# Performance work log

Measured on AMD Instinct MI355X. Metric: run time of the kernel, lower is better.

Reference implementation:

```python
import jax, jax.numpy as jnp
import numpy as np
from jax import lax

DN = ('NCHW', 'OIHW', 'NCHW')


def _conv(x, w, groups, pad):
    return lax.conv_general_dilated(x, w, (1, 1), ((pad, pad), (pad, pad)),
                                    dimension_numbers=DN, feature_group_count=groups)


def setup_inputs() -> dict:
    key = jax.random.key(0)
    k0, k1, k2, k3, k4 = jax.random.split(key, 5)
    B, C, H, W, O = 8, 192, 56, 56, 384
    x = jax.random.normal(k0, (B, C, H, W), jnp.float32)
    # torch init: normal(0, sqrt(2/n)), n = kh*kw*out_ch
    og_dw = jax.random.normal(k1, (C, 1, 3, 3), jnp.float32) * np.sqrt(2.0 / (9 * C))
    og_pw = jax.random.normal(k2, (18, C, 1, 1), jnp.float32) * np.sqrt(2.0 / 18)
    dcn_w = jax.random.normal(k3, (C, 1, 3, 3), jnp.float32) * np.sqrt(2.0 / (9 * C))
    pw_w = jax.random.normal(k4, (O, C, 1, 1), jnp.float32) * np.sqrt(2.0 / O)
    return {'x': x, 'og_dw': og_dw, 'og_pw': og_pw, 'dcn_w': dcn_w, 'pw_w': pw_w}


def _deform_sample(x, dy, dx):
    # x: [B,C,H,W]; dy,dx: [B,9,H,W] learned offsets. Returns [B,C,9,H,W]
    B, C, H, W = x.shape
    ky = (jnp.repeat(jnp.arange(3), 3) - 1).astype(x.dtype)   # tap row offsets
    kx = (jnp.tile(jnp.arange(3), 3) - 1).astype(x.dtype)     # tap col offsets
    gh = jnp.arange(H, dtype=x.dtype)[:, None]
    gw = jnp.arange(W, dtype=x.dtype)[None, :]
    ys = gh[None, None] + ky[None, :, None, None] + dy        # [B,9,H,W]
    xs = gw[None, None] + kx[None, :, None, None] + dx
    y0 = jnp.floor(ys)
    x0 = jnp.floor(xs)
    ty = ys - y0
    tx = xs - x0
    y0i = y0.astype(jnp.int32)
    x0i = x0.astype(jnp.int32)
    xf = x.reshape(B, C, H * W)
    gather = jax.vmap(lambda xb, ib: xb[:, ib])  # ([C,HW],[9,H,W]) -> [C,9,H,W]
    val = jnp.zeros((B, C, 9, H, W), x.dtype)
    corners = [(y0i, x0i, (1 - ty) * (1 - tx)),
               (y0i, x0i + 1, (1 - ty) * tx),
               (y0i + 1, x0i, ty * (1 - tx)),
               (y0i + 1, x0i + 1, ty * tx)]
    for yi, xi, wgt in corners:
        valid = ((yi >= 0) & (yi < H) & (xi >= 0) & (xi < W)).astype(x.dtype)
        idx = jnp.clip(yi, 0, H - 1) * W + jnp.clip(xi, 0, W - 1)  # [B,9,H,W]
        v = gather(xf, idx)                                        # [B,C,9,H,W]
        val = val + v * (wgt * valid)[:, None]
    return val


def reference(x, og_dw, og_pw, dcn_w, pw_w):
    B, C, H, W = x.shape
    O = pw_w.shape[0]
    # offset generator: depthwise 3x3 then 1x1 -> 18 channels, clamped
    off = _conv(_conv(x, og_dw, C, 1), og_pw, 1, 0)
    off = jnp.clip(off, -1.0, 1.0)
    off = off.reshape(B, 9, 2, H, W)
    dy, dx = off[:, :, 0], off[:, :, 1]
    # depthwise deformable conv 3x3
    val = _deform_sample(x, dy, dx)                       # [B,C,9,H,W]
    y = jnp.einsum('bckhw,ck->bchw', val, dcn_w.reshape(C, 9))
    # pointwise conv + Hardswish
    y = jnp.einsum('bchw,oc->bohw', y, pw_w.reshape(O, C))
    return y * jnp.clip(y + 3.0, 0.0, 6.0) / 6.0
```

## Files before the change

### kernel.cpp

```cpp
#include <hip/hip_runtime.h>

#define TPB 256
constexpr int B_ = 8, C_ = 192, H_ = 56, W_ = 56, O_ = 384;
constexpr int HW_ = H_ * W_;
constexpr int NOFF = 18;
constexpr int NPIX = B_ * HW_;
constexpr int K2 = 9 * C_;

typedef __attribute__((ext_vector_type(8))) short short8v;
typedef __attribute__((ext_vector_type(4))) float f32x4;

__device__ inline unsigned short f2bf(float f) {
  unsigned u = __builtin_bit_cast(unsigned, f);
  unsigned r = (u + 0x7fffu + ((u >> 16) & 1u)) >> 16;
  return (unsigned short)r;
}
__device__ inline float bflo(unsigned u) {
  return __builtin_bit_cast(float, u << 16);
}
__device__ inline float bfhi(unsigned u) {
  return __builtin_bit_cast(float, u & 0xffff0000u);
}

__global__ __launch_bounds__(TPB) void k_prep(const float* __restrict__ og_dw,
                                              const float* __restrict__ og_pw,
                                              const float* __restrict__ pw,
                                              unsigned short* __restrict__ wtb,
                                              unsigned short* __restrict__ w2b) {
  int i = blockIdx.x * TPB + threadIdx.x;
  if (i < O_ * C_) wtb[i] = f2bf(pw[i]);
  int j = i - O_ * C_;
  if (j >= 0 && j < 32 * K2) {
    int o = j / K2, k = j - o * K2;
    int tap = k / C_, c = k - tap * C_;
    float v = 0.f;
    if (o < NOFF) v = og_pw[o * C_ + c] * og_dw[c * 9 + tap];
    w2b[j] = f2bf(v);
  }
}

__global__ __launch_bounds__(TPB) void k_xt(const float* __restrict__ x,
                                            unsigned short* __restrict__ xt) {
  __shared__ unsigned short tile[64 * 198];
  int tid = threadIdx.x;
  int P0 = blockIdx.x * 64;
  int b = blockIdx.y;
#pragma unroll
  for (int i = 0; i < 48; ++i) {
    int idx = i * TPB + tid;
    int px = idx & 63;
    int c = idx >> 6;
    float v = x[((size_t)(b * C_ + c)) * HW_ + P0 + px];
    tile[px * 198 + c] = f2bf(v);
  }
  __syncthreads();
  unsigned* xtu = (unsigned*)xt;
#pragma unroll
  for (int i = 0; i < 24; ++i) {
    int d = i * TPB + tid;
    int px = d / 96;
    int c2 = d - px * 96;
    unsigned v = *(const unsigned*)&tile[px * 198 + c2 * 2];
    xtu[((size_t)b * HW_ + P0 + px) * 96 + c2] = v;
  }
}

__global__ __launch_bounds__(TPB) void k_off2s(const unsigned short* __restrict__ xt,
                                               const unsigned short* __restrict__ w2b,
                                               float* __restrict__ offp3) {
  __shared__ __align__(16) unsigned short hal[80 * 192];
  int tid = threadIdx.x;
  int w0 = blockIdx.x * 8;
  int h0 = blockIdx.y * 8;
  int bz = blockIdx.z;
  int b = bz & 7;
  int s = bz >> 3;
  int dy = s - 1;

  char* sb = (char*)hal;
  const uint4* xu4 = (const uint4*)xt;
#pragma unroll
  for (int i = 0; i < 8; ++i) {
    int u = i * TPB + tid;
    if (u < 1920) {
      int pos = u / 24, c4 = u - pos * 24;
      int ry = pos / 10;
      int gy = h0 + ry + dy;
      int gx = w0 - 1 + (pos - ry * 10);
      uint4 v = {0u, 0u, 0u, 0u};
      if ((unsigned)gy < (unsigned)H_ && (unsigned)gx < (unsigned)W_)
        v = xu4[((size_t)b * HW_ + gy * W_ + gx) * 24 + c4];
      *(uint4*)(sb + pos * 384 + ((c4 * 16) ^ ((pos & 7) << 4))) = v;
    }
  }
  __syncthreads();

  int wid = tid >> 6;
  int lane = tid & 63;
  int col = lane & 15;
  int kg = lane >> 4;
  int gpx = wid * 16 + col;
  int py = gpx >> 3, px_ = gpx & 7;

  f32x4 acc0 = (f32x4){0.f, 0.f, 0.f, 0.f};
  f32x4 acc1 = (f32x4){0.f, 0.f, 0.f, 0.f};

#pragma unroll
  for (int j = 0; j < 3; ++j) {
    int tap = 3 * s + j;
    int pos = py * 10 + px_ + j;
    int pbase = pos * 384;
    int psw = (pos & 7) << 4;
    const unsigned short* wrow = w2b + tap * C_ + kg * 8;
#pragma unroll
    for (int cs = 0; cs < 6; ++cs) {
      short8v bfrag = *(const short8v*)(sb + pbase + ((cs * 64 + kg * 16) ^ psw));
      short8v a0 = *(const short8v*)(wrow + cs * 32 + (size_t)col * K2);
      short8v a1 = *(const short8v*)(wrow + cs * 32 + (size_t)(16 + col) * K2);
      acc0 = __builtin_amdgcn_mfma_f32_16x16x32_bf16(a0, bfrag, acc0, 0, 0, 0);
      acc1 = __builtin_amdgcn_mfma_f32_16x16x32_bf16(a1, bfrag, acc1, 0, 0, 0);
    }
  }

  float* ob = offp3 + (size_t)(s * B_ + b) * NOFF * HW_ + (h0 + py) * W_ + w0 + px_;
#pragma unroll
  for (int reg = 0; reg < 4; ++reg) {
    int o0 = kg * 4 + reg;
    ob[(size_t)o0 * HW_] = acc0[reg];
    int o1 = 16 + kg * 4 + reg;
    if (o1 < NOFF) ob[(size_t)o1 * HW_] = acc1[reg];
  }
}

__global__ __launch_bounds__(TPB) void k_deform9s(const unsigned short* __restrict__ xt,
                                                  const float* __restrict__ offp3,
                                                  const float* __restrict__ dcn,
                                                  unsigned short* __restrict__ y1t) {
  __shared__ __align__(16) unsigned short hal[81 * 192];
  __shared__ __align__(16) float dcnT[9 * C_];
  int tid = threadIdx.x;
  int bid = blockIdx.x;
  int b = bid & 7;
  int tile = bid >> 3;
  int h0 = (tile / 14) * 4;
  int w0 = (tile - (tile / 14) * 14) * 4;

  for (int t = tid; t < 9 * C_; t += TPB) {
    int k = t / C_, c = t - k * C_;
    dcnT[t] = dcn[c * 9 + k];
  }
  char* sb = (char*)hal;
  const uint4* xu4 = (const uint4*)xt;
#pragma unroll
  for (int i = 0; i < 8; ++i) {
    int u = i * TPB + tid;
    if (u < 1944) {
      int pos = u / 24, c4 = u - pos * 24;
      int ly = pos / 9, lx = pos - ly * 9;
      int gy = h0 - 2 + ly, gx = w0 - 2 + lx;
      uint4 v = {0u, 0u, 0u, 0u};
      if ((unsigned)gy < (unsigned)H_ && (unsigned)gx < (unsigned)W_)
        v = xu4[((size_t)b * HW_ + gy * W_ + gx) * 24 + c4];
      *(uint4*)(sb + pos * 384 + ((c4 * 16) ^ ((pos & 7) << 4))) = v;
    }
  }
  __syncthreads();

  int pl = tid >> 4;
  int lg = tid & 15;
  int py = pl >> 2, px_ = pl & 3;
  int h = h0 + py, w = w0 + px_;
  int hw = h * W_ + w;
  const float* p0 = offp3 + (size_t)(0 * B_ + b) * NOFF * HW_ + hw;
  const float* p1 = offp3 + (size_t)(1 * B_ + b) * NOFF * HW_ + hw;
  const float* p2 = offp3 + (size_t)(2 * B_ + b) * NOFF * HW_ + hw;

  float acc[12];
#pragma unroll
  for (int j = 0; j < 12; ++j) acc[j] = 0.f;

#pragma unroll
  for (int tap = 0; tap < 9; ++tap) {
    int ky = tap / 3 - 1;
    int kx = tap - (tap / 3) * 3 - 1;
    size_t ody = (size_t)(2 * tap) * HW_;
    size_t odx = (size_t)(2 * tap + 1) * HW_;
    float dyv = p0[ody] + p1[ody] + p2[ody];
    float dxv = p0[odx] + p1[odx] + p2[odx];
    dyv = fminf(fmaxf(dyv, -1.f), 1.f);
    dxv = fminf(fmaxf(dxv, -1.f), 1.f);
    float ys = (float)(h + ky) + dyv;
    float xs = (float)(w + kx) + dxv;
    float y0f = floorf(ys), x0f = floorf(xs);
    float ty = ys - y0f, tx = xs - x0f;
    int y0 = (int)y0f, x0 = (int)x0f;
    float fy0 = ((unsigned)y0 < (unsigned)H_) ? 1.f : 0.f;
    float fy1 = ((unsigned)(y0 + 1) < (unsigned)H_) ? 1.f : 0.f;
    float fx0 = ((unsigned)x0 < (unsigned)W_) ? 1.f : 0.f;
    float fx1 = ((unsigned)(x0 + 1) < (unsigned)W_) ? 1.f : 0.f;
    float omty = 1.f - ty, omtx = 1.f - tx;
    float w00 = omty * omtx * fy0 * fx0;
    float w01 = omty * tx * fy0 * fx1;
    float w10 = ty * omtx * fy1 * fx0;
    float w11 = ty * tx * fy1 * fx1;
    int ly0 = y0 - (h0 - 2);
    int lx0 = x0 - (w0 - 2);
    int posA = ly0 * 9 + lx0;
    int pA = posA * 384, sA = (posA & 7) << 4;
    int pB = pA + 384, sB = ((posA + 1) & 7) << 4;
    int pC = pA + 9 * 384, sC = ((posA + 9) & 7) << 4;
    int pD = pC + 384, sD = ((posA + 10) & 7) << 4;
#pragma unroll
    for (int rep = 0; rep < 3; ++rep) {
      int bo = lg * 8 + rep * 128;
      uint2 u00 = *(const uint2*)(sb + pA + (bo ^ sA));
      uint2 u01 = *(const uint2*)(sb + pB + (bo ^ sB));
      uint2 u10 = *(const uint2*)(sb + pC + (bo ^ sC));
      uint2 u11 = *(const uint2*)(sb + pD + (bo ^ sD));
      f32x4 dw = *(const f32x4*)&dcnT[tap * C_ + lg * 4 + rep * 64];
      float s0 = w00 * bflo(u00.x) + w01 * bflo(u01.x) + w10 * bflo(u10.x) + w11 * bflo(u11.x);
      float s1 = w00 * bfhi(u00.x) + w01 * bfhi(u01.x) + w10 * bfhi(u10.x) + w11 * bfhi(u11.x);
      float s2 = w00 * bflo(u00.y) + w01 * bflo(u01.y) + w10 * bflo(u10.y) + w11 * bflo(u11.y);
      float s3 = w00 * bfhi(u00.y) + w01 * bfhi(u01.y) + w10 * bfhi(u10.y) + w11 * bfhi(u11.y);
      acc[rep * 4 + 0] += s0 * dw.x;
      acc[rep * 4 + 1] += s1 * dw.y;
      acc[rep * 4 + 2] += s2 * dw.z;
      acc[rep * 4 + 3] += s3 * dw.w;
    }
  }

  size_t ob = ((size_t)b * HW_ + hw) * C_ + lg * 4;
#pragma unroll
  for (int rep = 0; rep < 3; ++rep) {
    uint2 pk;
    pk.x = (unsigned)f2bf(acc[rep * 4 + 0]) | ((unsigned)f2bf(acc[rep * 4 + 1]) << 16);
    pk.y = (unsigned)f2bf(acc[rep * 4 + 2]) | ((unsigned)f2bf(acc[rep * 4 + 3]) << 16);
    *(uint2*)(y1t + ob + rep * 64) = pk;
  }
}

__global__ __launch_bounds__(TPB) void k_gemm4(const unsigned short* __restrict__ y1t,
                                               const unsigned short* __restrict__ wtb,
                                               float* __restrict__ out) {
  __shared__ __align__(16) unsigned short bsm[64 * 192];
  int tid = threadIdx.x;
  int n0 = blockIdx.x * 64;
  int mbase = blockIdx.y * 192;

  const uint4* src = (const uint4*)(y1t + (size_t)n0 * C_);
  char* sbase = (char*)bsm;
#pragma unroll
  for (int i = 0; i < 6; ++i) {
    int u = i * TPB + tid;
    int row = u / 24;
    int c4 = u - row * 24;
    uint4 v = src[u];
    *(uint4*)(sbase + row * 384 + ((c4 * 16) ^ ((row & 7) << 4))) = v;
  }
  __syncthreads();

  int wid = tid >> 6;
  int lane = tid & 63;
  int col = lane & 15;
  int kg = lane >> 4;
  int wr = wid >> 1;
  int wc = wid & 1;

#pragma unroll 1
  for (int mi = 0; mi < 3; ++mi) {
    int m0 = mbase + mi * 64;
    f32x4 acc[2][2];
#pragma unroll
    for (int mf = 0; mf < 2; ++mf)
#pragma unroll
      for (int nf = 0; nf < 2; ++nf) acc[mf][nf] = (f32x4){0.f, 0.f, 0.f, 0.f};

#pragma unroll
    for (int k0 = 0; k0 < C_; k0 += 32) {
      short8v a[2], bfr[2];
#pragma unroll
      for (int mf = 0; mf < 2; ++mf)
        a[mf] = *(const short8v*)(wtb + (m0 + wr * 32 + mf * 16 + col) * C_ + k0 + kg * 8);
#pragma unroll
      for (int nf = 0; nf < 2; ++nf) {
        int brow = wc * 32 + nf * 16 + col;
        int kb = (k0 + kg * 8) * 2;
        bfr[nf] = *(const short8v*)(sbase + brow * 384 + (kb ^ ((brow & 7) << 4)));
      }
#pragma unroll
      for (int mf = 0; mf < 2; ++mf)
#pragma unroll
        for (int nf = 0; nf < 2; ++nf)
          acc[mf][nf] = __builtin_amdgcn_mfma_f32_16x16x32_bf16(a[mf], bfr[nf], acc[mf][nf], 0, 0, 0);
    }

#pragma unroll
    for (int mf = 0; mf < 2; ++mf) {
#pragma unroll
      for (int nf = 0; nf < 2; ++nf) {
        int p = n0 + wc * 32 + nf * 16 + col;
        int bb = p / HW_;
        int hw = p - bb * HW_;
#pragma unroll
        for (int reg = 0; reg < 4; ++reg) {
          int o = m0 + wr * 32 + mf * 16 + kg * 4 + reg;
          float a = acc[mf][nf][reg];
          float r = a * fminf(fmaxf(a + 3.f, 0.f), 6.f) * (1.f / 6.f);
          out[((size_t)bb * O_ + o) * HW_ + hw] = r;
        }
      }
    }
  }
}

extern "C" void kernel_launch(void* const* d_in, const int* in_sizes, int n_in,
                              void* d_out, int out_size, void* d_ws, size_t ws_size,
                              hipStream_t stream) {
  const float* x = (const float*)d_in[0];
  const float* og_dw = (const float*)d_in[1];
  const float* og_pw = (const float*)d_in[2];
  const float* dcn_w = (const float*)d_in[3];
  const float* pw_w = (const float*)d_in[4];
  float* out = (float*)d_out;

  float* ws = (float*)d_ws;
  float* offp3 = ws;
  unsigned short* y1t = (unsigned short*)(offp3 + 3 * (size_t)B_ * NOFF * HW_);
  unsigned short* wtb = y1t + (size_t)NPIX * C_;
  unsigned short* x_t = wtb + (size_t)O_ * C_;
  unsigned short* w2b = x_t + (size_t)NPIX * C_;

  k_prep<<<(O_ * C_ + 32 * K2 + TPB - 1) / TPB, TPB, 0, stream>>>(og_dw, og_pw, pw_w, wtb, w2b);
  k_xt<<<dim3(HW_ / 64, B_), TPB, 0, stream>>>(x, x_t);
  k_off2s<<<dim3(W_ / 8, H_ / 8, B_ * 3), TPB, 0, stream>>>(x_t, w2b, offp3);
  k_deform9s<<<196 * B_, TPB, 0, stream>>>(x_t, offp3, dcn_w, y1t);
  k_gemm4<<<dim3(NPIX / 64, 2), TPB, 0, stream>>>(y1t, wtb, out);
}
```

Before: 93.92 us.

## Enlarge deform tile to 4x8 with shared bilinear weight table

The deformable sampling kernel now processes 4x8 pixel tiles with 512 threads, so the loaded halo (13x8 plus borders) has less overlap overhead per pixel. Bilinear weights and corner positions are computed once per (pixel, tap) by 288 threads, stored in shared memory as fp16, and then read by all channel lanes instead of being recomputed by each of the 16 lanes. The transposed depthwise weights are precomputed once in the prep kernel and read from global memory, so each block no longer builds them in shared memory. The cost is more shared memory per block and fp16 rounding of the interpolation weights.

```diff
diff --git a/kernel.cpp b/kernel.cpp
--- a/kernel.cpp
+++ b/kernel.cpp
@@ -1,4 +1,5 @@
 #include <hip/hip_runtime.h>
+#include <hip/hip_fp16.h>
 
 #define TPB 256
 constexpr int B_ = 8, C_ = 192, H_ = 56, W_ = 56, O_ = 384;
@@ -21,12 +22,20 @@
 __device__ inline float bfhi(unsigned u) {
   return __builtin_bit_cast(float, u & 0xffff0000u);
 }
+__device__ inline unsigned short f2h(float f) {
+  return __half_as_ushort(__float2half(f));
+}
+__device__ inline float h2f(unsigned short u) {
+  return __half2float(__ushort_as_half(u));
+}
 
 __global__ __launch_bounds__(TPB) void k_prep(const float* __restrict__ og_dw,
                                               const float* __restrict__ og_pw,
                                               const float* __restrict__ pw,
+                                              const float* __restrict__ dcn,
                                               unsigned short* __restrict__ wtb,
-                                              unsigned short* __restrict__ w2b) {
+                                              unsigned short* __restrict__ w2b,
+                                              float* __restrict__ dcnT_g) {
   int i = blockIdx.x * TPB + threadIdx.x;
   if (i < O_ * C_) wtb[i] = f2bf(pw[i]);
   int j = i - O_ * C_;
@@ -36,6 +45,11 @@
     float v = 0.f;
     if (o < NOFF) v = og_pw[o * C_ + c] * og_dw[c * 9 + tap];
     w2b[j] = f2bf(v);
+  }
+  int j2 = i - O_ * C_ - 32 * K2;
+  if (j2 >= 0 && j2 < 9 * C_) {
+    int k = j2 / C_, c = j2 - k * C_;
+    dcnT_g[j2] = dcn[c * 9 + k];
   }
 }
 
@@ -132,31 +146,28 @@
   }
 }
 
-__global__ __launch_bounds__(TPB) void k_deform9s(const unsigned short* __restrict__ xt,
-                                                  const float* __restrict__ offp3,
-                                                  const float* __restrict__ dcn,
-                                                  unsigned short* __restrict__ y1t) {
-  __shared__ __align__(16) unsigned short hal[81 * 192];
-  __shared__ __align__(16) float dcnT[9 * C_];
+__global__ __launch_bounds__(512, 8) void k_deform10(const unsigned short* __restrict__ xt,
+                                                     const float* __restrict__ offp3,
+                                                     const float* __restrict__ dcnT_g,
+                                                     unsigned short* __restrict__ y1t) {
+  __shared__ __align__(16) unsigned short hal[117 * 192];
+  __shared__ __align__(16) unsigned wtab[32 * 9 * 4];
   int tid = threadIdx.x;
   int bid = blockIdx.x;
   int b = bid & 7;
   int tile = bid >> 3;
-  int h0 = (tile / 14) * 4;
-  int w0 = (tile - (tile / 14) * 14) * 4;
-
-  for (int t = tid; t < 9 * C_; t += TPB) {
-    int k = t / C_, c = t - k * C_;
-    dcnT[t] = dcn[c * 9 + k];
-  }
+  int ty = tile / 7;
+  int h0 = ty * 4;
+  int w0 = (tile - ty * 7) * 8;
+
   char* sb = (char*)hal;
   const uint4* xu4 = (const uint4*)xt;
 #pragma unroll
-  for (int i = 0; i < 8; ++i) {
-    int u = i * TPB + tid;
-    if (u < 1944) {
+  for (int i = 0; i < 6; ++i) {
+    int u = i * 512 + tid;
+    if (u < 2808) {
       int pos = u / 24, c4 = u - pos * 24;
-      int ly = pos / 9, lx = pos - ly * 9;
+      int ly = pos / 13, lx = pos - ly * 13;
       int gy = h0 - 2 + ly, gx = w0 - 2 + lx;
       uint4 v = {0u, 0u, 0u, 0u};
       if ((unsigned)gy < (unsigned)H_ && (unsigned)gx < (unsigned)W_)
@@ -164,27 +175,19 @@
       *(uint4*)(sb + pos * 384 + ((c4 * 16) ^ ((pos & 7) << 4))) = v;
     }
   }
-  __syncthreads();
-
-  int pl = tid >> 4;
-  int lg = tid & 15;
-  int py = pl >> 2, px_ = pl & 3;
-  int h = h0 + py, w = w0 + px_;
-  int hw = h * W_ + w;
-  const float* p0 = offp3 + (size_t)(0 * B_ + b) * NOFF * HW_ + hw;
-  const float* p1 = offp3 + (size_t)(1 * B_ + b) * NOFF * HW_ + hw;
-  const float* p2 = offp3 + (size_t)(2 * B_ + b) * NOFF * HW_ + hw;
-
-  float acc[12];
-#pragma unroll
-  for (int j = 0; j < 12; ++j) acc[j] = 0.f;
-
-#pragma unroll
-  for (int tap = 0; tap < 9; ++tap) {
-    int ky = tap / 3 - 1;
-    int kx = tap - (tap / 3) * 3 - 1;
+
+  if (tid < 288) {
+    int pxl = tid / 9, tap = tid - pxl * 9;
+    int py = pxl >> 3, pxx = pxl & 7;
+    int h = h0 + py, w = w0 + pxx;
+    int hw = h * W_ + w;
+    const float* p0 = offp3 + (size_t)b * NOFF * HW_ + hw;
+    const float* p1 = p0 + (size_t)B_ * NOFF * HW_;
+    const float* p2 = p1 + (size_t)B_ * NOFF * HW_;
+    int t3 = tap / 3;
+    int ky = t3 - 1, kx = tap - t3 * 3 - 1;
     size_t ody = (size_t)(2 * tap) * HW_;
-    size_t odx = (size_t)(2 * tap + 1) * HW_;
+    size_t odx = ody + HW_;
     float dyv = p0[ody] + p1[ody] + p2[ody];
     float dxv = p0[odx] + p1[odx] + p2[odx];
     dyv = fminf(fmaxf(dyv, -1.f), 1.f);
@@ -192,24 +195,48 @@
     float ys = (float)(h + ky) + dyv;
     float xs = (float)(w + kx) + dxv;
     float y0f = floorf(ys), x0f = floorf(xs);
-    float ty = ys - y0f, tx = xs - x0f;
+    float tyf = ys - y0f, txf = xs - x0f;
     int y0 = (int)y0f, x0 = (int)x0f;
     float fy0 = ((unsigned)y0 < (unsigned)H_) ? 1.f : 0.f;
     float fy1 = ((unsigned)(y0 + 1) < (unsigned)H_) ? 1.f : 0.f;
     float fx0 = ((unsigned)x0 < (unsigned)W_) ? 1.f : 0.f;
     float fx1 = ((unsigned)(x0 + 1) < (unsigned)W_) ? 1.f : 0.f;
-    float omty = 1.f - ty, omtx = 1.f - tx;
+    float omty = 1.f - tyf, omtx = 1.f - txf;
     float w00 = omty * omtx * fy0 * fx0;
-    float w01 = omty * tx * fy0 * fx1;
-    float w10 = ty * omtx * fy1 * fx0;
-    float w11 = ty * tx * fy1 * fx1;
-    int ly0 = y0 - (h0 - 2);
-    int lx0 = x0 - (w0 - 2);
-    int posA = ly0 * 9 + lx0;
+    float w01 = omty * txf * fy0 * fx1;
+    float w10 = tyf * omtx * fy1 * fx0;
+    float w11 = tyf * txf * fy1 * fx1;
+    int posA = (y0 - (h0 - 2)) * 13 + (x0 - (w0 - 2));
+    uint4 e;
+    e.x = (unsigned)f2h(w00) | ((unsigned)f2h(w01) << 16);
+    e.y = (unsigned)f2h(w10) | ((unsigned)f2h(w11) << 16);
+    e.z = (unsigned)posA;
+    e.w = 0u;
+    *(uint4*)&wtab[(size_t)tid * 4] = e;
+  }
+  __syncthreads();
+
+  int pl = tid >> 4;
+  int lg = tid & 15;
+  int py = pl >> 3, pxx = pl & 7;
+  int hw = (h0 + py) * W_ + w0 + pxx;
+
+  float acc[12];
+#pragma unroll
+  for (int j = 0; j < 12; ++j) acc[j] = 0.f;
+
+#pragma unroll
+  for (int tap = 0; tap < 9; ++tap) {
+    uint4 e = *(const uint4*)&wtab[(size_t)(pl * 9 + tap) * 4];
+    float w00 = h2f((unsigned short)(e.x & 0xffffu));
+    float w01 = h2f((unsigned short)(e.x >> 16));
+    float w10 = h2f((unsigned short)(e.y & 0xffffu));
+    float w11 = h2f((unsigned short)(e.y >> 16));
+    int posA = (int)e.z;
     int pA = posA * 384, sA = (posA & 7) << 4;
     int pB = pA + 384, sB = ((posA + 1) & 7) << 4;
-    int pC = pA + 9 * 384, sC = ((posA + 9) & 7) << 4;
-    int pD = pC + 384, sD = ((posA + 10) & 7) << 4;
+    int pC = pA + 13 * 384, sC = ((posA + 13) & 7) << 4;
+    int pD = pC + 384, sD = ((posA + 14) & 7) << 4;
 #pragma unroll
     for (int rep = 0; rep < 3; ++rep) {
       int bo = lg * 8 + rep * 128;
@@ -217,7 +244,7 @@
       uint2 u01 = *(const uint2*)(sb + pB + (bo ^ sB));
       uint2 u10 = *(const uint2*)(sb + pC + (bo ^ sC));
       uint2 u11 = *(const uint2*)(sb + pD + (bo ^ sD));
-      f32x4 dw = *(const f32x4*)&dcnT[tap * C_ + lg * 4 + rep * 64];
+      f32x4 dw = *(const f32x4*)&dcnT_g[tap * C_ + lg * 4 + rep * 64];
       float s0 = w00 * bflo(u00.x) + w01 * bflo(u01.x) + w10 * bflo(u10.x) + w11 * bflo(u11.x);
       float s1 = w00 * bfhi(u00.x) + w01 * bfhi(u01.x) + w10 * bfhi(u10.x) + w11 * bfhi(u11.x);
       float s2 = w00 * bflo(u00.y) + w01 * bflo(u01.y) + w10 * bflo(u10.y) + w11 * bflo(u11.y);
@@ -325,14 +352,16 @@
 
   float* ws = (float*)d_ws;
   float* offp3 = ws;
-  unsigned short* y1t = (unsigned short*)(offp3 + 3 * (size_t)B_ * NOFF * HW_);
+  float* dcnT_g = offp3 + 3 * (size_t)B_ * NOFF * HW_;
+  unsigned short* y1t = (unsigned short*)(dcnT_g + 9 * C_);
   unsigned short* wtb = y1t + (size_t)NPIX * C_;
   unsigned short* x_t = wtb + (size_t)O_ * C_;
   unsigned short* w2b = x_t + (size_t)NPIX * C_;
 
-  k_prep<<<(O_ * C_ + 32 * K2 + TPB - 1) / TPB, TPB, 0, stream>>>(og_dw, og_pw, pw_w, wtb, w2b);
+  k_prep<<<(O_ * C_ + 32 * K2 + 9 * C_ + TPB - 1) / TPB, TPB, 0, stream>>>(
+      og_dw, og_pw, pw_w, dcn_w, wtb, w2b, dcnT_g);
   k_xt<<<dim3(HW_ / 64, B_), TPB, 0, stream>>>(x, x_t);
   k_off2s<<<dim3(W_ / 8, H_ / 8, B_ * 3), TPB, 0, stream>>>(x_t, w2b, offp3);
-  k_deform9s<<<196 * B_, TPB, 0, stream>>>(x_t, offp3, dcn_w, y1t);
+  k_deform10<<<196 * 4 * B_ / 8, 512, 0, stream>>>(x_t, offp3, dcnT_g, y1t);
   k_gemm4<<<dim3(NPIX / 64, 2), TPB, 0, stream>>>(y1t, wtb, out);
 }
```

Measured after the change: 87.73 us. 1.07x faster.
